# Performance work log

Measured on AMD Instinct MI355X. Metric: run time of the kernel, lower is better.

Reference implementation:

```python
import jax, jax.numpy as jnp
import numpy as np

T, N, E = 48, 1000, 32000
D_IN, H = 32, 64


def setup_inputs() -> dict:
    key = jax.random.key(0)
    ks = jax.random.split(key, 14)
    p = lambda k, s: (jax.random.normal(k, s, dtype=jnp.float32) * 0.05)
    return {
        "x": jax.random.normal(ks[0], (T, N, D_IN), dtype=jnp.float32),
        "edge_index": jax.random.randint(ks[1], (2, E), 0, N, dtype=jnp.int32),
        "hidden_state": jnp.zeros((N, H), jnp.float32),
        "cell_state": jnp.zeros((N, H), jnp.float32),
        # GCNConv 1 (lin weight stored as [in, out] so x @ W matches x @ lin.weight.T)
        "Wg1": p(ks[2], (D_IN, H)), "bg1": p(ks[3], (H,)),
        # GCNConv 2
        "Wg2": p(ks[4], (H, H)), "bg2": p(ks[5], (H,)),
        # LSTMCell params, torch gate order (i, f, g, o)
        "W_ih": p(ks[6], (4 * H, H)), "W_hh": p(ks[7], (4 * H, H)),
        "b_ih": p(ks[8], (4 * H,)), "b_hh": p(ks[9], (4 * H,)),
        # final Linear(hidden_dim * num_nodes -> num_nodes)
        "W_lin": p(ks[10], (N, H * N)), "b_lin": p(ks[11], (N,)),
    }


def _gcn_norm(edge_index, num_nodes):
    """PyG GCNConv default: add self loops, symmetric D^-1/2 (A+I) D^-1/2 norm."""
    loops = jnp.arange(num_nodes, dtype=edge_index.dtype)
    src = jnp.concatenate([edge_index[0], loops])
    dst = jnp.concatenate([edge_index[1], loops])
    deg = jax.ops.segment_sum(jnp.ones(src.shape[0], jnp.float32), dst,
                              num_segments=num_nodes)
    dinv = jax.lax.rsqrt(jnp.maximum(deg, 1.0))  # self loops guarantee deg >= 1
    norm = dinv[src] * dinv[dst]
    return src, dst, norm


def _gcn(x, W, b, src, dst, norm, num_nodes):
    x = x @ W                              # [N, out]
    msg = x[src] * norm[:, None]           # gather + scale  [E+N, out]
    return jax.ops.segment_sum(msg, dst, num_segments=num_nodes) + b


def reference(x, edge_index, hidden_state, cell_state,
              Wg1, bg1, Wg2, bg2, W_ih, W_hh, b_ih, b_hh, W_lin, b_lin):
    src, dst, norm = _gcn_norm(edge_index, N)

    def step(carry, xt):
        h, c = carry
        g = jax.nn.relu(_gcn(xt, Wg1, bg1, src, dst, norm, N))
        g = _gcn(g, Wg2, bg2, src, dst, norm, N)
        gates = g @ W_ih.T + b_ih + h @ W_hh.T + b_hh   # [N, 4H]
        i, f, gg, o = jnp.split(gates, 4, axis=-1)
        c = jax.nn.sigmoid(f) * c + jax.nn.sigmoid(i) * jnp.tanh(gg)
        h = jax.nn.sigmoid(o) * jnp.tanh(c)
        return (h, c), h

    (hidden_state, cell_state), h_seq = jax.lax.scan(step, (hidden_state, cell_state), x)
    flat = h_seq.reshape(T, N * H)                      # view(-1, hidden*num_nodes)
    out = flat @ W_lin.T + b_lin                        # [T, N]
    out = out.reshape(-1, N, 4)                         # [T/4, N, 4]
    return out, hidden_state, cell_state
```

## Files before the change

kernel.cpp:

```cpp
#include <hip/hip_runtime.h>
#include <math.h>

#define T_STEPS 48
#define N_NODES 1000
#define E_EDGES 32000
#define DIN     32
#define H_DIM   64

#define O_INDEG  0
#define O_FILL   1024
#define O_ROWPTR 2048
#define O_CSRC   4096
#define O_CNORM  36864
#define O_DINV   69632
#define O_SELF   70656
#define O_BUF0   71680
#define O_BUF1   (71680 + 3072000)
#define O_HSB    (71680 + 6144000)
#define WS_NEED_HSB ((size_t)(O_HSB + 1536000) * 4)

typedef __attribute__((ext_vector_type(8))) short short8;
typedef __attribute__((ext_vector_type(4))) float f32x4;
typedef __attribute__((ext_vector_type(4))) unsigned int uint32x4;

__device__ __forceinline__ float sigmf(float v) { return 1.0f / (1.0f + __expf(-v)); }

__global__ void k_zero(int* __restrict__ p) { p[blockIdx.x * 256 + threadIdx.x] = 0; }

__global__ void k_count(const int* __restrict__ ei, int* __restrict__ indeg) {
  int e = blockIdx.x * 256 + threadIdx.x;
  if (e < E_EDGES) atomicAdd(&indeg[ei[E_EDGES + e]], 1);
}

__global__ void k_scan(const int* __restrict__ indeg, int* __restrict__ rowptr,
                       float* __restrict__ dinv, float* __restrict__ selfn) {
  __shared__ int sdat[1024];
  int tid = threadIdx.x;
  int v = (tid < N_NODES) ? indeg[tid] : 0;
  sdat[tid] = v;
  __syncthreads();
  for (int off = 1; off < 1024; off <<= 1) {
    int add = (tid >= off) ? sdat[tid - off] : 0;
    __syncthreads();
    sdat[tid] += add;
    __syncthreads();
  }
  if (tid < N_NODES) {
    rowptr[tid + 1] = sdat[tid];
    float di = rsqrtf((float)(v + 1));
    dinv[tid] = di;
    selfn[tid] = di * di;
  }
  if (tid == 0) rowptr[0] = 0;
}

__global__ void k_scatter(const int* __restrict__ ei, const int* __restrict__ rowptr,
                          int* __restrict__ fill, const float* __restrict__ dinv,
                          int* __restrict__ csrc, float* __restrict__ cnorm) {
  int e = blockIdx.x * 256 + threadIdx.x;
  if (e >= E_EDGES) return;
  int s = ei[e], d = ei[E_EDGES + e];
  int pos = atomicAdd(&fill[d], 1);
  int idx = rowptr[d] + pos;
  csrc[idx] = s;
  cnorm[idx] = dinv[s] * dinv[d];
}

__global__ void __launch_bounds__(256) k_t1(const float* __restrict__ x,
                                            const float* __restrict__ Wg1,
                                            float* __restrict__ T1) {
  __shared__ float sWT[H_DIM * 36];
  __shared__ float sx[4][DIN];
  const int tid = threadIdx.x, wv = tid >> 6, h = tid & 63;
  for (int i = tid; i < DIN * H_DIM; i += 256) sWT[(i & 63) * 36 + (i >> 6)] = Wg1[i];
  __syncthreads();
  const int r0 = blockIdx.x * 64 + wv * 16;
  const float4* wrow = (const float4*)&sWT[h * 36];
  for (int it = 0; it < 16; ++it) {
    const int r = r0 + it;
    if (h < DIN) sx[wv][h] = x[r * DIN + h];
    float acc = 0.f;
    const float4* xp = (const float4*)&sx[wv][0];
#pragma unroll
    for (int k4 = 0; k4 < 8; ++k4) {
      float4 xv = xp[k4], wv4 = wrow[k4];
      acc += xv.x * wv4.x + xv.y * wv4.y + xv.z * wv4.z + xv.w * wv4.w;
    }
    T1[r * H_DIM + h] = acc;
  }
}

__device__ __forceinline__ float gath_node(const float* __restrict__ Tsrc,
                                           const int* __restrict__ es,
                                           const float* __restrict__ ew,
                                           int cnt, int h) {
  float a0 = 0.f, a1 = 0.f, a2 = 0.f, a3 = 0.f;
  float a4 = 0.f, a5 = 0.f, a6 = 0.f, a7 = 0.f;
  int e = 0;
  if (cnt >= 8) {
    float p0 = Tsrc[es[0] * 64 + h], p1 = Tsrc[es[1] * 64 + h];
    float p2 = Tsrc[es[2] * 64 + h], p3 = Tsrc[es[3] * 64 + h];
    float p4 = Tsrc[es[4] * 64 + h], p5 = Tsrc[es[5] * 64 + h];
    float p6 = Tsrc[es[6] * 64 + h], p7 = Tsrc[es[7] * 64 + h];
    for (e = 8; e + 8 <= cnt; e += 8) {
      float n0 = Tsrc[es[e + 0] * 64 + h], n1 = Tsrc[es[e + 1] * 64 + h];
      float n2 = Tsrc[es[e + 2] * 64 + h], n3 = Tsrc[es[e + 3] * 64 + h];
      float n4 = Tsrc[es[e + 4] * 64 + h], n5 = Tsrc[es[e + 5] * 64 + h];
      float n6 = Tsrc[es[e + 6] * 64 + h], n7 = Tsrc[es[e + 7] * 64 + h];
      a0 += ew[e - 8] * p0; a1 += ew[e - 7] * p1;
      a2 += ew[e - 6] * p2; a3 += ew[e - 5] * p3;
      a4 += ew[e - 4] * p4; a5 += ew[e - 3] * p5;
      a6 += ew[e - 2] * p6; a7 += ew[e - 1] * p7;
      p0 = n0; p1 = n1; p2 = n2; p3 = n3; p4 = n4; p5 = n5; p6 = n6; p7 = n7;
    }
    a0 += ew[e - 8] * p0; a1 += ew[e - 7] * p1;
    a2 += ew[e - 6] * p2; a3 += ew[e - 5] * p3;
    a4 += ew[e - 4] * p4; a5 += ew[e - 3] * p5;
    a6 += ew[e - 2] * p6; a7 += ew[e - 1] * p7;
  }
  for (; e < cnt; ++e) a0 += ew[e] * Tsrc[es[e] * 64 + h];
  return ((a0 + a1) + (a2 + a3)) + ((a4 + a5) + (a6 + a7));
}

#define ECHUNK 768
__global__ void __launch_bounds__(256) k_gath(const float* __restrict__ Tall,
                                              const float* __restrict__ bias,
                                              const int* __restrict__ rowptr,
                                              const int* __restrict__ csrc,
                                              const float* __restrict__ cnorm,
                                              const float* __restrict__ selfn,
                                              float* __restrict__ Dall, int relu) {
  __shared__ int   s_src[ECHUNK];
  __shared__ float s_wt[ECHUNK];
  __shared__ float sb[64];
  const int tid = threadIdx.x, wv = tid >> 6, h = tid & 63;
  if (tid < 64) sb[tid] = bias[tid];
  const int t = blockIdx.x >> 6, nb16 = (blockIdx.x & 63) * 16;
  if (nb16 >= N_NODES) return;
  const float* Tsrc = Tall + t * 64000;
  float* dst = Dall + t * 64000;
  const int nE = (nb16 + 16 < N_NODES) ? nb16 + 16 : N_NODES;
  const int r0 = rowptr[nb16], r1 = rowptr[nE];
  const int tot = r1 - r0;
  const bool fits = (tot <= ECHUNK);
  if (fits)
    for (int i = tid; i < tot; i += 256) { s_src[i] = csrc[r0 + i]; s_wt[i] = cnorm[r0 + i]; }
  __syncthreads();
  for (int i = 0; i < 4; ++i) {
    const int n = nb16 + wv * 4 + i;
    if (n >= N_NODES) continue;
    const int a = rowptr[n], b = rowptr[n + 1];
    float acc = selfn[n] * Tsrc[n * 64 + h];
    if (fits) {
      acc += gath_node(Tsrc, s_src + (a - r0), s_wt + (a - r0), b - a, h);
    } else {
      for (int e = a; e < b; ++e) acc += cnorm[e] * Tsrc[csrc[e] * 64 + h];
    }
    acc += sb[h];
    if (relu) acc = fmaxf(acc, 0.f);
    dst[n * 64 + h] = acc;
  }
}

__global__ void __launch_bounds__(256) k_mm2(const float* __restrict__ G1,
                                             const float* __restrict__ Wg2,
                                             float* __restrict__ T2) {
  __shared__ float sW[H_DIM * H_DIM];
  __shared__ float sx[4][H_DIM];
  const int tid = threadIdx.x, wv = tid >> 6, h = tid & 63;
  for (int i = tid; i < H_DIM * H_DIM; i += 256) sW[i] = Wg2[i];
  __syncthreads();
  const int r0 = blockIdx.x * 64 + wv * 16;
  for (int it = 0; it < 16; ++it) {
    const int r = r0 + it;
    sx[wv][h] = G1[r * 64 + h];
    float acc = 0.f;
#pragma unroll
    for (int k = 0; k < H_DIM; ++k) acc += sx[wv][k] * sW[k * H_DIM + h];
    T2[r * 64 + h] = acc;
  }
}

__global__ void __launch_bounds__(256) k_lstm(const float* __restrict__ G2,
                                              const float* __restrict__ h0,
                                              const float* __restrict__ c0,
                                              const float* __restrict__ Wih,
                                              const float* __restrict__ Whh,
                                              const float* __restrict__ bih,
                                              const float* __restrict__ bhh,
                                              float* __restrict__ hsg,
                                              unsigned short* __restrict__ hsb,
                                              float* __restrict__ outp) {
  const int tid = threadIdx.x, nb = blockIdx.x;
  __shared__ float sh[64];
  __shared__ float sg2[2][64];
  __shared__ float sgates[256];
  float4 Wih4[16], Whh4[16];
  {
    const float4* wp = (const float4*)(Wih + tid * H_DIM);
    const float4* vp = (const float4*)(Whh + tid * H_DIM);
#pragma unroll
    for (int k = 0; k < 16; ++k) { Wih4[k] = wp[k]; Whh4[k] = vp[k]; }
  }
  const float bsum = bih[tid] + bhh[tid];
  float creg = 0.f;
  if (tid < 64) {
    sh[tid] = h0[nb * 64 + tid];
    creg = c0[nb * 64 + tid];
    sg2[0][tid] = G2[nb * 64 + tid];
  }
  __syncthreads();
  for (int t = 0; t < T_STEPS; ++t) {
    const int cur = t & 1;
    float gnext = 0.f;
    if (t < T_STEPS - 1 && tid < 64) gnext = G2[(t + 1) * 64000 + nb * 64 + tid];
    float gv = bsum;
    const float4* gp = (const float4*)&sg2[cur][0];
    const float4* hp = (const float4*)sh;
#pragma unroll
    for (int k = 0; k < 16; ++k) {
      float4 a = gp[k], b = hp[k];
      gv += a.x * Wih4[k].x + a.y * Wih4[k].y + a.z * Wih4[k].z + a.w * Wih4[k].w;
      gv += b.x * Whh4[k].x + b.y * Whh4[k].y + b.z * Whh4[k].z + b.w * Whh4[k].w;
    }
    sgates[tid] = gv;
    __syncthreads();
    if (tid < 64) {
      float iv = sgates[tid], fv = sgates[64 + tid], gg = sgates[128 + tid], ov = sgates[192 + tid];
      float cn = sigmf(fv) * creg + sigmf(iv) * tanhf(gg);
      float hn = sigmf(ov) * tanhf(cn);
      creg = cn;
      sh[tid] = hn;
      if (hsb) {
        unsigned u = __float_as_uint(hn);
        u += 0x7fff + ((u >> 16) & 1);
        hsb[t * 64000 + nb * 64 + tid] = (unsigned short)(u >> 16);
      } else {
        hsg[t * 64000 + nb * 64 + tid] = hn;
      }
      if (t < T_STEPS - 1) sg2[cur ^ 1][tid] = gnext;
    }
    __syncthreads();
  }
  if (tid < 64) {
    outp[48000 + nb * 64 + tid] = sh[tid];
    outp[48000 + 64000 + nb * 64 + tid] = creg;
  }
}

__global__ void k_cvt(const float* __restrict__ src, unsigned* __restrict__ dst) {
  const int id = blockIdx.x * 256 + threadIdx.x;
  const float4 v = ((const float4*)src)[id];
  unsigned lo, hi;
  asm("v_cvt_pk_bf16_f32 %0, %1, %2" : "=v"(lo) : "v"(v.x), "v"(v.y));
  asm("v_cvt_pk_bf16_f32 %0, %1, %2" : "=v"(hi) : "v"(v.z), "v"(v.w));
  ((uint2*)dst)[id] = make_uint2(lo, hi);
}

#define GS_KC 40
__global__ void __launch_bounds__(256) k_gemmS(const unsigned short* __restrict__ hsb,
                                               const float* __restrict__ Wlin,
                                               float* __restrict__ part) {
  __shared__ float4 red[4][3][64];
  const int tid = threadIdx.x;
  const int kc = blockIdx.x % GS_KC, nt = blockIdx.x / GS_KC;
  const int wv = tid >> 6, l = tid & 63;
  const int lr = l & 15, kg = l >> 4;
  const int kcbase = kc * 1600;

  const unsigned short* ap0 = hsb + (size_t)(0  + lr) * 64000 + kcbase + kg * 8 + wv * 32;
  const unsigned short* ap1 = hsb + (size_t)(16 + lr) * 64000 + kcbase + kg * 8 + wv * 32;
  const unsigned short* ap2 = hsb + (size_t)(32 + lr) * 64000 + kcbase + kg * 8 + wv * 32;
  int nrow = nt * 16 + lr; if (nrow > N_NODES - 1) nrow = N_NODES - 1;
  const float* bp = Wlin + (size_t)nrow * 64000 + kcbase + kg * 8 + wv * 32;

  f32x4 acc0 = {0.f, 0.f, 0.f, 0.f}, acc1 = acc0, acc2 = acc0;

  for (int s = wv; s < 50; s += 4) {
    const short8 a0 = *(const short8*)ap0;
    const short8 a1 = *(const short8*)ap1;
    const short8 a2 = *(const short8*)ap2;
    const float4 b0 = *(const float4*)bp;
    const float4 b1 = *(const float4*)(bp + 4);
    unsigned p0, p1, p2, p3;
    asm("v_cvt_pk_bf16_f32 %0, %1, %2" : "=v"(p0) : "v"(b0.x), "v"(b0.y));
    asm("v_cvt_pk_bf16_f32 %0, %1, %2" : "=v"(p1) : "v"(b0.z), "v"(b0.w));
    asm("v_cvt_pk_bf16_f32 %0, %1, %2" : "=v"(p2) : "v"(b1.x), "v"(b1.y));
    asm("v_cvt_pk_bf16_f32 %0, %1, %2" : "=v"(p3) : "v"(b1.z), "v"(b1.w));
    uint32x4 bu = {p0, p1, p2, p3};
    const short8 bs = __builtin_bit_cast(short8, bu);
    acc0 = __builtin_amdgcn_mfma_f32_16x16x32_bf16(a0, bs, acc0, 0, 0, 0);
    acc1 = __builtin_amdgcn_mfma_f32_16x16x32_bf16(a1, bs, acc1, 0, 0, 0);
    acc2 = __builtin_amdgcn_mfma_f32_16x16x32_bf16(a2, bs, acc2, 0, 0, 0);
    ap0 += 128; ap1 += 128; ap2 += 128; bp += 128;
  }

  red[wv][0][l] = make_float4(acc0[0], acc0[1], acc0[2], acc0[3]);
  red[wv][1][l] = make_float4(acc1[0], acc1[1], acc1[2], acc1[3]);
  red[wv][2][l] = make_float4(acc2[0], acc2[1], acc2[2], acc2[3]);
  __syncthreads();
  if (wv < 3) {
    const float4 r0 = red[0][wv][l], r1 = red[1][wv][l];
    const float4 r2 = red[2][wv][l], r3 = red[3][wv][l];
    const float4 s4 = make_float4(r0.x + r1.x + r2.x + r3.x,
                                  r0.y + r1.y + r2.y + r3.y,
                                  r0.z + r1.z + r2.z + r3.z,
                                  r0.w + r1.w + r2.w + r3.w);
    const int n = nt * 16 + lr;
    if (n < N_NODES) {
      const int trow = wv * 16 + kg * 4;
      float* base = part + (size_t)(kc * 48 + trow) * 1000 + n;
      base[0]    = s4.x;
      base[1000] = s4.y;
      base[2000] = s4.z;
      base[3000] = s4.w;
    }
  }
}

__global__ void __launch_bounds__(256) k_gemmM(const unsigned short* __restrict__ hsb,
                                               const float* __restrict__ Wlin,
                                               float* __restrict__ part) {
  const int tid = threadIdx.x;
  const int kc = blockIdx.x & 15, nt = blockIdx.x >> 4;
  const int wv = tid >> 6, l = tid & 63;
  const int lr = l & 15, kg = l >> 4;
  const int kcbase = kc * 4000;
  const int kp = kc * 4 + wv;

  const unsigned short* ap0 = hsb + (size_t)(0  + lr) * 64000 + kcbase + kg * 8 + wv * 32;
  const unsigned short* ap1 = hsb + (size_t)(16 + lr) * 64000 + kcbase + kg * 8 + wv * 32;
  const unsigned short* ap2 = hsb + (size_t)(32 + lr) * 64000 + kcbase + kg * 8 + wv * 32;
  int nrow = nt * 16 + lr; if (nrow > N_NODES - 1) nrow = N_NODES - 1;
  const float* bp = Wlin + (size_t)nrow * 64000 + kcbase + kg * 8 + wv * 32;

  f32x4 acc0 = {0.f, 0.f, 0.f, 0.f}, acc1 = acc0, acc2 = acc0;

  for (int s = wv; s < 125; s += 4) {
    const short8 a0 = *(const short8*)ap0;
    const short8 a1 = *(const short8*)ap1;
    const short8 a2 = *(const short8*)ap2;
    const float4 b0 = *(const float4*)bp;
    const float4 b1 = *(const float4*)(bp + 4);
    unsigned p0, p1, p2, p3;
    asm("v_cvt_pk_bf16_f32 %0, %1, %2" : "=v"(p0) : "v"(b0.x), "v"(b0.y));
    asm("v_cvt_pk_bf16_f32 %0, %1, %2" : "=v"(p1) : "v"(b0.z), "v"(b0.w));
    asm("v_cvt_pk_bf16_f32 %0, %1, %2" : "=v"(p2) : "v"(b1.x), "v"(b1.y));
    asm("v_cvt_pk_bf16_f32 %0, %1, %2" : "=v"(p3) : "v"(b1.z), "v"(b1.w));
    uint32x4 bu = {p0, p1, p2, p3};
    const short8 bs = __builtin_bit_cast(short8, bu);
    acc0 = __builtin_amdgcn_mfma_f32_16x16x32_bf16(a0, bs, acc0, 0, 0, 0);
    acc1 = __builtin_amdgcn_mfma_f32_16x16x32_bf16(a1, bs, acc1, 0, 0, 0);
    acc2 = __builtin_amdgcn_mfma_f32_16x16x32_bf16(a2, bs, acc2, 0, 0, 0);
    ap0 += 128; ap1 += 128; ap2 += 128; bp += 128;
  }

  const int n = nt * 16 + lr;
  if (n < N_NODES) {
    const int trow = kg * 4;
    float* base = part + (size_t)(kp * 48) * 1000 + n;
#pragma unroll
    for (int j = 0; j < 4; ++j) base[(0  + trow + j) * 1000] = acc0[j];
#pragma unroll
    for (int j = 0; j < 4; ++j) base[(16 + trow + j) * 1000] = acc1[j];
#pragma unroll
    for (int j = 0; j < 4; ++j) base[(32 + trow + j) * 1000] = acc2[j];
  }
}

__global__ void k_reduce(const float* __restrict__ part, const float* __restrict__ blin,
                         float* __restrict__ outp, int np) {
  const int id = blockIdx.x * 256 + threadIdx.x;
  if (id >= T_STEPS * N_NODES) return;
  const int t = id / N_NODES, n = id - t * N_NODES;
  float s = blin[n];
  for (int kp = 0; kp < np; ++kp) s += part[(size_t)(kp * 48 + t) * 1000 + n];
  outp[id] = s;
}

extern "C" void kernel_launch(void* const* d_in, const int* in_sizes, int n_in,
                              void* d_out, int out_size, void* d_ws, size_t ws_size,
                              hipStream_t stream) {
  const float* x    = (const float*)d_in[0];
  const int*   ei   = (const int*)d_in[1];
  const float* h0   = (const float*)d_in[2];
  const float* c0   = (const float*)d_in[3];
  const float* Wg1  = (const float*)d_in[4];
  const float* bg1  = (const float*)d_in[5];
  const float* Wg2  = (const float*)d_in[6];
  const float* bg2  = (const float*)d_in[7];
  const float* Wih  = (const float*)d_in[8];
  const float* Whh  = (const float*)d_in[9];
  const float* bih  = (const float*)d_in[10];
  const float* bhh  = (const float*)d_in[11];
  const float* Wlin = (const float*)d_in[12];
  const float* blin = (const float*)d_in[13];
  float* outp = (float*)d_out;
  float* wsf  = (float*)d_ws;
  int*   wsi  = (int*)d_ws;

  int*   indeg  = wsi + O_INDEG;
  int*   fill   = wsi + O_FILL;
  int*   rowptr = wsi + O_ROWPTR;
  int*   csrc   = wsi + O_CSRC;
  float* cnorm  = wsf + O_CNORM;
  float* dinv   = wsf + O_DINV;
  float* selfn  = wsf + O_SELF;
  float* buf0   = wsf + O_BUF0;
  float* buf1   = wsf + O_BUF1;

  const bool big = ws_size >= WS_NEED_HSB;

  k_zero<<<8, 256, 0, stream>>>(wsi);
  k_count<<<(E_EDGES + 255) / 256, 256, 0, stream>>>(ei, indeg);
  k_scan<<<1, 1024, 0, stream>>>(indeg, rowptr, dinv, selfn);
  k_scatter<<<(E_EDGES + 255) / 256, 256, 0, stream>>>(ei, rowptr, fill, dinv, csrc, cnorm);

  k_t1<<<750, 256, 0, stream>>>(x, Wg1, buf0);
  k_gath<<<3072, 256, 0, stream>>>(buf0, bg1, rowptr, csrc, cnorm, selfn, buf1, 1);
  k_mm2<<<750, 256, 0, stream>>>(buf1, Wg2, buf0);
  k_gath<<<3072, 256, 0, stream>>>(buf0, bg2, rowptr, csrc, cnorm, selfn, buf1, 0);

  if (big) {
    unsigned short* hsb = (unsigned short*)(wsf + O_HSB);
    k_lstm<<<1000, 256, 0, stream>>>(buf1, h0, c0, Wih, Whh, bih, bhh,
                                     buf0, hsb, outp);
    k_gemmS<<<GS_KC * 63, 256, 0, stream>>>(hsb, Wlin, buf0);
    k_reduce<<<(T_STEPS * N_NODES + 255) / 256, 256, 0, stream>>>(buf0, blin, outp, GS_KC);
  } else {
    k_lstm<<<1000, 256, 0, stream>>>(buf1, h0, c0, Wih, Whh, bih, bhh,
                                     buf0, (unsigned short*)nullptr, outp);
    k_cvt<<<3000, 256, 0, stream>>>(buf0, (unsigned*)buf1);
    k_gemmM<<<16 * 63, 256, 0, stream>>>((const unsigned short*)buf1, Wlin, buf0);
    k_reduce<<<(T_STEPS * N_NODES + 255) / 256, 256, 0, stream>>>(buf0, blin, outp, 64);
  }
}
```

Before: 358.8 us.

## Fuse graph setup into one kernel and reduce final GEMM via atomics

Merges the four CSR-building kernels (zero, degree count, scan, scatter) into a single 1024-thread block that works in shared memory, removing three launches and the global atomics on the degree and fill counters. The big-workspace path also drops the separate reduction kernel: the LSTM kernel seeds the output with the bias and the split-K GEMM adds its partial sums straight into the output with float atomics. The cost is nondeterministic float summation order, atomic contention on the 48x1000 output, and edge processing that now runs serially on one block.

```diff
diff --git a/kernel.cpp b/kernel.cpp
--- a/kernel.cpp
+++ b/kernel.cpp
@@ -7,8 +7,6 @@
 #define DIN     32
 #define H_DIM   64
 
-#define O_INDEG  0
-#define O_FILL   1024
 #define O_ROWPTR 2048
 #define O_CSRC   4096
 #define O_CNORM  36864
@@ -25,45 +23,47 @@
 
 __device__ __forceinline__ float sigmf(float v) { return 1.0f / (1.0f + __expf(-v)); }
 
-__global__ void k_zero(int* __restrict__ p) { p[blockIdx.x * 256 + threadIdx.x] = 0; }
-
-__global__ void k_count(const int* __restrict__ ei, int* __restrict__ indeg) {
-  int e = blockIdx.x * 256 + threadIdx.x;
-  if (e < E_EDGES) atomicAdd(&indeg[ei[E_EDGES + e]], 1);
-}
-
-__global__ void k_scan(const int* __restrict__ indeg, int* __restrict__ rowptr,
-                       float* __restrict__ dinv, float* __restrict__ selfn) {
-  __shared__ int sdat[1024];
-  int tid = threadIdx.x;
-  int v = (tid < N_NODES) ? indeg[tid] : 0;
-  sdat[tid] = v;
+__global__ void __launch_bounds__(1024) k_setup(const int* __restrict__ ei,
+                                                int* __restrict__ rowptr,
+                                                int* __restrict__ csrc,
+                                                float* __restrict__ cnorm,
+                                                float* __restrict__ dinv,
+                                                float* __restrict__ selfn) {
+  __shared__ int   s_deg[1024];
+  __shared__ int   s_fill[1000];
+  __shared__ int   s_scan[1024];
+  __shared__ float s_dinv[1000];
+  const int tid = threadIdx.x;
+  s_deg[tid] = 0;
+  if (tid < N_NODES) s_fill[tid] = 0;
+  __syncthreads();
+  for (int e = tid; e < E_EDGES; e += 1024) atomicAdd(&s_deg[ei[E_EDGES + e]], 1);
+  __syncthreads();
+  const int v = (tid < N_NODES) ? s_deg[tid] : 0;
+  s_scan[tid] = v;
   __syncthreads();
   for (int off = 1; off < 1024; off <<= 1) {
-    int add = (tid >= off) ? sdat[tid - off] : 0;
+    int add = (tid >= off) ? s_scan[tid - off] : 0;
     __syncthreads();
-    sdat[tid] += add;
+    s_scan[tid] += add;
     __syncthreads();
   }
   if (tid < N_NODES) {
-    rowptr[tid + 1] = sdat[tid];
-    float di = rsqrtf((float)(v + 1));
+    rowptr[tid + 1] = s_scan[tid];
+    const float di = rsqrtf((float)(v + 1));
     dinv[tid] = di;
     selfn[tid] = di * di;
+    s_dinv[tid] = di;
   }
   if (tid == 0) rowptr[0] = 0;
-}
-
-__global__ void k_scatter(const int* __restrict__ ei, const int* __restrict__ rowptr,
-                          int* __restrict__ fill, const float* __restrict__ dinv,
-                          int* __restrict__ csrc, float* __restrict__ cnorm) {
-  int e = blockIdx.x * 256 + threadIdx.x;
-  if (e >= E_EDGES) return;
-  int s = ei[e], d = ei[E_EDGES + e];
-  int pos = atomicAdd(&fill[d], 1);
-  int idx = rowptr[d] + pos;
-  csrc[idx] = s;
-  cnorm[idx] = dinv[s] * dinv[d];
+  __syncthreads();
+  for (int e = tid; e < E_EDGES; e += 1024) {
+    const int s = ei[e], d = ei[E_EDGES + e];
+    const int pos = atomicAdd(&s_fill[d], 1);
+    const int base = (d == 0) ? 0 : s_scan[d - 1];
+    csrc[base + pos] = s;
+    cnorm[base + pos] = s_dinv[s] * s_dinv[d];
+  }
 }
 
 __global__ void __launch_bounds__(256) k_t1(const float* __restrict__ x,
@@ -188,13 +188,15 @@
                                               const float* __restrict__ Whh,
                                               const float* __restrict__ bih,
                                               const float* __restrict__ bhh,
+                                              const float* __restrict__ blin,
                                               float* __restrict__ hsg,
                                               unsigned short* __restrict__ hsb,
-                                              float* __restrict__ outp) {
+                                              float* __restrict__ outp, int initout) {
   const int tid = threadIdx.x, nb = blockIdx.x;
   __shared__ float sh[64];
   __shared__ float sg2[2][64];
   __shared__ float sgates[256];
+  if (initout && tid < T_STEPS) outp[tid * N_NODES + nb] = blin[nb];
   float4 Wih4[16], Whh4[16];
   {
     const float4* wp = (const float4*)(Wih + tid * H_DIM);
@@ -260,7 +262,7 @@
 #define GS_KC 40
 __global__ void __launch_bounds__(256) k_gemmS(const unsigned short* __restrict__ hsb,
                                                const float* __restrict__ Wlin,
-                                               float* __restrict__ part) {
+                                               float* __restrict__ outp) {
   __shared__ float4 red[4][3][64];
   const int tid = threadIdx.x;
   const int kc = blockIdx.x % GS_KC, nt = blockIdx.x / GS_KC;
@@ -309,11 +311,11 @@
     const int n = nt * 16 + lr;
     if (n < N_NODES) {
       const int trow = wv * 16 + kg * 4;
-      float* base = part + (size_t)(kc * 48 + trow) * 1000 + n;
-      base[0]    = s4.x;
-      base[1000] = s4.y;
-      base[2000] = s4.z;
-      base[3000] = s4.w;
+      float* base = outp + (size_t)trow * 1000 + n;
+      atomicAdd(&base[0],    s4.x);
+      atomicAdd(&base[1000], s4.y);
+      atomicAdd(&base[2000], s4.z);
+      atomicAdd(&base[3000], s4.w);
     }
   }
 }
@@ -399,8 +401,6 @@
   float* wsf  = (float*)d_ws;
   int*   wsi  = (int*)d_ws;
 
-  int*   indeg  = wsi + O_INDEG;
-  int*   fill   = wsi + O_FILL;
   int*   rowptr = wsi + O_ROWPTR;
   int*   csrc   = wsi + O_CSRC;
   float* cnorm  = wsf + O_CNORM;
@@ -411,10 +411,7 @@
 
   const bool big = ws_size >= WS_NEED_HSB;
 
-  k_zero<<<8, 256, 0, stream>>>(wsi);
-  k_count<<<(E_EDGES + 255) / 256, 256, 0, stream>>>(ei, indeg);
-  k_scan<<<1, 1024, 0, stream>>>(indeg, rowptr, dinv, selfn);
-  k_scatter<<<(E_EDGES + 255) / 256, 256, 0, stream>>>(ei, rowptr, fill, dinv, csrc, cnorm);
+  k_setup<<<1, 1024, 0, stream>>>(ei, rowptr, csrc, cnorm, dinv, selfn);
 
   k_t1<<<750, 256, 0, stream>>>(x, Wg1, buf0);
   k_gath<<<3072, 256, 0, stream>>>(buf0, bg1, rowptr, csrc, cnorm, selfn, buf1, 1);
@@ -423,13 +420,12 @@
 
   if (big) {
     unsigned short* hsb = (unsigned short*)(wsf + O_HSB);
-    k_lstm<<<1000, 256, 0, stream>>>(buf1, h0, c0, Wih, Whh, bih, bhh,
-                                     buf0, hsb, outp);
-    k_gemmS<<<GS_KC * 63, 256, 0, stream>>>(hsb, Wlin, buf0);
-    k_reduce<<<(T_STEPS * N_NODES + 255) / 256, 256, 0, stream>>>(buf0, blin, outp, GS_KC);
+    k_lstm<<<1000, 256, 0, stream>>>(buf1, h0, c0, Wih, Whh, bih, bhh, blin,
+                                     buf0, hsb, outp, 1);
+    k_gemmS<<<GS_KC * 63, 256, 0, stream>>>(hsb, Wlin, outp);
   } else {
-    k_lstm<<<1000, 256, 0, stream>>>(buf1, h0, c0, Wih, Whh, bih, bhh,
-                                     buf0, (unsigned short*)nullptr, outp);
+    k_lstm<<<1000, 256, 0, stream>>>(buf1, h0, c0, Wih, Whh, bih, bhh, blin,
+                                     buf0, (unsigned short*)nullptr, outp, 0);
     k_cvt<<<3000, 256, 0, stream>>>(buf0, (unsigned*)buf1);
     k_gemmM<<<16 * 63, 256, 0, stream>>>((const unsigned short*)buf1, Wlin, buf0);
     k_reduce<<<(T_STEPS * N_NODES + 255) / 256, 256, 0, stream>>>(buf0, blin, outp, 64);
```

After: 418.3 us. +16.6%, slower.

## Replace sparse GCN gather with dense MFMA normalized-adjacency matmul

Applied to the files above, without the earlier changes.

Materializes the normalized adjacency as a dense 1000x1024 matrix, split into bf16 hi and lo parts, and computes each GCN aggregation as a dense bf16 MFMA GEMM against transposed bf16 features. This replaces the irregular CSR gather kernels with regular tensor-core work and adds a transpose kernel per layer. It trades about 32x more arithmetic for dense, coalesced access. Features are rounded to bf16, which costs accuracy. Building the dense matrix does an O(N*deg) scan per node, and entries beyond 512 edges per node are silently dropped.

```diff
diff --git a/kernel.cpp b/kernel.cpp
--- a/kernel.cpp
+++ b/kernel.cpp
@@ -17,13 +17,20 @@
 #define O_BUF0   71680
 #define O_BUF1   (71680 + 3072000)
 #define O_HSB    (71680 + 6144000)
-#define WS_NEED_HSB ((size_t)(O_HSB + 1536000) * 4)
+#define O_SHI    (O_HSB + 1536000)
+#define O_SLO    (O_SHI + 516096)
+#define O_TT     (O_SLO + 516096)
+#define WS_NEED_BIG ((size_t)(O_TT + 1572864) * 4)
 
 typedef __attribute__((ext_vector_type(8))) short short8;
 typedef __attribute__((ext_vector_type(4))) float f32x4;
 typedef __attribute__((ext_vector_type(4))) unsigned int uint32x4;
 
 __device__ __forceinline__ float sigmf(float v) { return 1.0f / (1.0f + __expf(-v)); }
+__device__ __forceinline__ unsigned short bf16rne(float f) {
+  unsigned u = __float_as_uint(f);
+  return (unsigned short)((u + 0x7fff + ((u >> 16) & 1)) >> 16);
+}
 
 __global__ void k_zero(int* __restrict__ p) { p[blockIdx.x * 256 + threadIdx.x] = 0; }
 
@@ -64,6 +71,88 @@
   int idx = rowptr[d] + pos;
   csrc[idx] = s;
   cnorm[idx] = dinv[s] * dinv[d];
+}
+
+__global__ void __launch_bounds__(256) k_sden(const int* __restrict__ rowptr,
+                                              const int* __restrict__ csrc,
+                                              const float* __restrict__ cnorm,
+                                              const float* __restrict__ selfn,
+                                              unsigned short* __restrict__ Shi,
+                                              unsigned short* __restrict__ Slo) {
+  __shared__ int   es[512];
+  __shared__ float ew[512];
+  const int n = blockIdx.x;
+  const int tid = threadIdx.x;
+  int cnt = 0;
+  if (n < N_NODES) {
+    const int a = rowptr[n], b = rowptr[n + 1];
+    cnt = b - a; if (cnt > 512) cnt = 512;
+    for (int i = tid; i < cnt; i += 256) { es[i] = csrc[a + i]; ew[i] = cnorm[a + i]; }
+  }
+  __syncthreads();
+  for (int c = tid; c < 1024; c += 256) {
+    float s = 0.f;
+    if (n < N_NODES) {
+      if (c == n) s = selfn[n];
+      for (int e = 0; e < cnt; ++e) if (es[e] == c) s += ew[e];
+    }
+    const unsigned short hb = bf16rne(s);
+    const float hf = __uint_as_float(((unsigned)hb) << 16);
+    Shi[n * 1024 + c] = hb;
+    Slo[n * 1024 + c] = bf16rne(s - hf);
+  }
+}
+
+__global__ void __launch_bounds__(256) k_tr(const float* __restrict__ T,
+                                            unsigned short* __restrict__ Tt) {
+  __shared__ float lds[128][65];
+  const int t = blockIdx.x >> 3, mc = (blockIdx.x & 7) * 128;
+  const int tid = threadIdx.x;
+  for (int i = tid; i < 2048; i += 256) {
+    const int m = i >> 4, h4 = (i & 15) * 4;
+    const int gm = mc + m;
+    float4 v = make_float4(0.f, 0.f, 0.f, 0.f);
+    if (gm < N_NODES) v = *(const float4*)&T[(size_t)(t * 1000 + gm) * 64 + h4];
+    lds[m][h4] = v.x; lds[m][h4 + 1] = v.y; lds[m][h4 + 2] = v.z; lds[m][h4 + 3] = v.w;
+  }
+  __syncthreads();
+  for (int i = tid; i < 8192; i += 256) {
+    const int h = i >> 7, m = i & 127;
+    Tt[((size_t)t * 64 + h) * 1024 + mc + m] = bf16rne(lds[m][h]);
+  }
+}
+
+__global__ void __launch_bounds__(256) k_gmfa(const unsigned short* __restrict__ Shi,
+                                              const unsigned short* __restrict__ Slo,
+                                              const unsigned short* __restrict__ Tt,
+                                              const float* __restrict__ bias,
+                                              float* __restrict__ G, int relu) {
+  const int t = blockIdx.x / 63, ntile = blockIdx.x % 63;
+  const int tid = threadIdx.x, wv = tid >> 6, l = tid & 63;
+  const int lr = l & 15, kg = l >> 4;
+  const unsigned short* ah = Shi + (size_t)(ntile * 16 + lr) * 1024 + kg * 8;
+  const unsigned short* al = Slo + (size_t)(ntile * 16 + lr) * 1024 + kg * 8;
+  const unsigned short* bp = Tt + ((size_t)t * 64 + wv * 16 + lr) * 1024 + kg * 8;
+  f32x4 acc = {0.f, 0.f, 0.f, 0.f};
+#pragma unroll 4
+  for (int ks = 0; ks < 32; ++ks) {
+    const short8 aH = *(const short8*)(ah + ks * 32);
+    const short8 aL = *(const short8*)(al + ks * 32);
+    const short8 b  = *(const short8*)(bp + ks * 32);
+    acc = __builtin_amdgcn_mfma_f32_16x16x32_bf16(aH, b, acc, 0, 0, 0);
+    acc = __builtin_amdgcn_mfma_f32_16x16x32_bf16(aL, b, acc, 0, 0, 0);
+  }
+  const int h = wv * 16 + lr;
+  const float bv = bias[h];
+#pragma unroll
+  for (int j = 0; j < 4; ++j) {
+    const int n = ntile * 16 + kg * 4 + j;
+    if (n < N_NODES) {
+      float v = acc[j] + bv;
+      if (relu) v = fmaxf(v, 0.f);
+      G[(size_t)t * 64000 + n * 64 + h] = v;
+    }
+  }
 }
 
 __global__ void __launch_bounds__(256) k_t1(const float* __restrict__ x,
@@ -232,9 +321,7 @@
       creg = cn;
       sh[tid] = hn;
       if (hsb) {
-        unsigned u = __float_as_uint(hn);
-        u += 0x7fff + ((u >> 16) & 1);
-        hsb[t * 64000 + nb * 64 + tid] = (unsigned short)(u >> 16);
+        hsb[t * 64000 + nb * 64 + tid] = bf16rne(hn);
       } else {
         hsg[t * 64000 + nb * 64 + tid] = hn;
       }
@@ -409,25 +496,35 @@
   float* buf0   = wsf + O_BUF0;
   float* buf1   = wsf + O_BUF1;
 
-  const bool big = ws_size >= WS_NEED_HSB;
+  const bool big = ws_size >= WS_NEED_BIG;
 
   k_zero<<<8, 256, 0, stream>>>(wsi);
   k_count<<<(E_EDGES + 255) / 256, 256, 0, stream>>>(ei, indeg);
   k_scan<<<1, 1024, 0, stream>>>(indeg, rowptr, dinv, selfn);
   k_scatter<<<(E_EDGES + 255) / 256, 256, 0, stream>>>(ei, rowptr, fill, dinv, csrc, cnorm);
 
-  k_t1<<<750, 256, 0, stream>>>(x, Wg1, buf0);
-  k_gath<<<3072, 256, 0, stream>>>(buf0, bg1, rowptr, csrc, cnorm, selfn, buf1, 1);
-  k_mm2<<<750, 256, 0, stream>>>(buf1, Wg2, buf0);
-  k_gath<<<3072, 256, 0, stream>>>(buf0, bg2, rowptr, csrc, cnorm, selfn, buf1, 0);
-
   if (big) {
+    unsigned short* Shi = (unsigned short*)(wsf + O_SHI);
+    unsigned short* Slo = (unsigned short*)(wsf + O_SLO);
+    unsigned short* Tt  = (unsigned short*)(wsf + O_TT);
     unsigned short* hsb = (unsigned short*)(wsf + O_HSB);
+
+    k_sden<<<1008, 256, 0, stream>>>(rowptr, csrc, cnorm, selfn, Shi, Slo);
+    k_t1<<<750, 256, 0, stream>>>(x, Wg1, buf0);
+    k_tr<<<384, 256, 0, stream>>>(buf0, Tt);
+    k_gmfa<<<48 * 63, 256, 0, stream>>>(Shi, Slo, Tt, bg1, buf1, 1);
+    k_mm2<<<750, 256, 0, stream>>>(buf1, Wg2, buf0);
+    k_tr<<<384, 256, 0, stream>>>(buf0, Tt);
+    k_gmfa<<<48 * 63, 256, 0, stream>>>(Shi, Slo, Tt, bg2, buf1, 0);
     k_lstm<<<1000, 256, 0, stream>>>(buf1, h0, c0, Wih, Whh, bih, bhh,
                                      buf0, hsb, outp);
     k_gemmS<<<GS_KC * 63, 256, 0, stream>>>(hsb, Wlin, buf0);
     k_reduce<<<(T_STEPS * N_NODES + 255) / 256, 256, 0, stream>>>(buf0, blin, outp, GS_KC);
   } else {
+    k_t1<<<750, 256, 0, stream>>>(x, Wg1, buf0);
+    k_gath<<<3072, 256, 0, stream>>>(buf0, bg1, rowptr, csrc, cnorm, selfn, buf1, 1);
+    k_mm2<<<750, 256, 0, stream>>>(buf1, Wg2, buf0);
+    k_gath<<<3072, 256, 0, stream>>>(buf0, bg2, rowptr, csrc, cnorm, selfn, buf1, 0);
     k_lstm<<<1000, 256, 0, stream>>>(buf1, h0, c0, Wih, Whh, bih, bhh,
                                      buf0, (unsigned short*)nullptr, outp);
     k_cvt<<<3000, 256, 0, stream>>>(buf0, (unsigned*)buf1);
```

Measured after the change: 561.4 us. +56.5%, slower.
